# Performance work log

Measured on AMD Instinct MI355X. Metric: run time of the kernel, lower is better.

## Reference

```python
import jax, jax.numpy as jnp
import numpy as np

D_ENC = 512
D_DEC = 512
D_JOINT = D_ENC + D_DEC  # 1024
V = 1024


def setup_inputs() -> dict:
    key = jax.random.key(0)
    ks = jax.random.split(key, 8)
    s = lambda fan_in: 1.0 / np.sqrt(fan_in)
    return {
        "encoder_output": jax.random.normal(ks[0], (8, 200, D_ENC), dtype=jnp.float32),
        "decoder_output": jax.random.normal(ks[1], (8, 50, D_DEC), dtype=jnp.float32),
        "W_enc": jax.random.uniform(ks[2], (D_JOINT, D_ENC), jnp.float32, -s(D_ENC), s(D_ENC)),
        "b_enc": jax.random.uniform(ks[3], (D_JOINT,), jnp.float32, -s(D_ENC), s(D_ENC)),
        "W_dec": jax.random.uniform(ks[4], (D_JOINT, D_DEC), jnp.float32, -s(D_DEC), s(D_DEC)),
        "b_dec": jax.random.uniform(ks[5], (D_JOINT,), jnp.float32, -s(D_DEC), s(D_DEC)),
        "W_fc": jax.random.uniform(ks[6], (V, D_JOINT), jnp.float32, -s(D_JOINT), s(D_JOINT)),
        "b_fc": jax.random.uniform(ks[7], (V,), jnp.float32, -s(D_JOINT), s(D_JOINT)),
    }


def reference(encoder_output, decoder_output, W_enc, b_enc, W_dec, b_dec, W_fc, b_fc):
    # enc: (B, T, D_JOINT); dec: (B, U, D_JOINT)
    enc = jnp.einsum('btd,jd->btj', encoder_output, W_enc) + b_enc
    dec = jnp.einsum('bud,jd->buj', decoder_output, W_dec) + b_dec
    # broadcast join: (B, T, U, D_JOINT)
    combined = enc[:, :, None, :] + dec[:, None, :, :]
    logits = jnp.einsum('btuj,vj->btuv', jnp.tanh(combined), W_fc) + b_fc
    return jax.nn.log_softmax(logits, axis=-1)
```

## Files before the change

### kernel.cpp

```cpp
#include <hip/hip_runtime.h>
#include <hip/hip_bf16.h>
#include <hip/hip_fp8.h>

#define TT 200
#define UU 50
#define BB 8
#define DJ 1024
#define DE 512
#define VV 1024
#define M_TOTAL (BB*TT*UU)
#define MB 80
#define NITER 32
#define WINV (1.0f/32.0f)

typedef float f32x4 __attribute__((ext_vector_type(4)));

__device__ __forceinline__ float fast_tanh(float x) {
    float e = __expf(2.f * x);
    return 1.f - 2.f / (e + 1.f);
}

__device__ __forceinline__ unsigned char f2fp8(float x) {
    return __hip_fp8_e4m3(x).__x;
}

__device__ __forceinline__ unsigned long long tanh_pack_fp8(float4 e0, float4 e1, float4 d0, float4 d1) {
    unsigned long long r;
    r  = (unsigned long long)f2fp8(fast_tanh(e0.x + d0.x));
    r |= (unsigned long long)f2fp8(fast_tanh(e0.y + d0.y)) << 8;
    r |= (unsigned long long)f2fp8(fast_tanh(e0.z + d0.z)) << 16;
    r |= (unsigned long long)f2fp8(fast_tanh(e0.w + d0.w)) << 24;
    r |= (unsigned long long)f2fp8(fast_tanh(e1.x + d1.x)) << 32;
    r |= (unsigned long long)f2fp8(fast_tanh(e1.y + d1.y)) << 40;
    r |= (unsigned long long)f2fp8(fast_tanh(e1.z + d1.z)) << 48;
    r |= (unsigned long long)f2fp8(fast_tanh(e1.w + d1.w)) << 56;
    return r;
}

__global__ __launch_bounds__(256) void k_prep(const float* __restrict__ enc,
                                              const float* __restrict__ dec,
                                              const float* __restrict__ W_enc,
                                              const float* __restrict__ b_enc,
                                              const float* __restrict__ W_dec,
                                              const float* __restrict__ b_dec,
                                              const float* __restrict__ W_fc,
                                              float* __restrict__ encp,
                                              float* __restrict__ decp,
                                              unsigned char* __restrict__ wfc8) {
    const int bx = blockIdx.x, by = blockIdx.y;
    const int tid = threadIdx.x;
    if (bx >= 125) {
        const int wid = (bx - 125) * 4 + by;
        #pragma unroll
        for (int r = 0; r < 2; ++r) {
            const int G = wid * 512 + r * 256 + tid;
            const int gk = G >> 10, n = G & 1023;
            const float* src = W_fc + (size_t)n * DJ + gk * 8;
            float4 a = *(const float4*)(src);
            float4 b = *(const float4*)(src + 4);
            unsigned long long rr;
            rr  = (unsigned long long)f2fp8(a.x * 32.f);
            rr |= (unsigned long long)f2fp8(a.y * 32.f) << 8;
            rr |= (unsigned long long)f2fp8(a.z * 32.f) << 16;
            rr |= (unsigned long long)f2fp8(a.w * 32.f) << 24;
            rr |= (unsigned long long)f2fp8(b.x * 32.f) << 32;
            rr |= (unsigned long long)f2fp8(b.y * 32.f) << 40;
            rr |= (unsigned long long)f2fp8(b.z * 32.f) << 48;
            rr |= (unsigned long long)f2fp8(b.w * 32.f) << 56;
            *(unsigned long long*)(wfc8 + (size_t)G * 8) = rr;
        }
        return;
    }
    __shared__ float in_s[16][DE];
    const bool isDec = bx >= 100;
    const float* in  = isDec ? dec   : enc;
    const float* W   = isDec ? W_dec : W_enc;
    const float* bia = isDec ? b_dec : b_enc;
    float* out       = isDec ? decp  : encp;
    const int NR     = isDec ? (BB*UU) : (BB*TT);
    const int m0 = (isDec ? (bx - 100) : bx) * 16;
    #pragma unroll
    for (int it = 0; it < 8; ++it) {
        int idx = tid + it * 256;
        int r = idx >> 7, c = (idx & 127) << 2;
        *(float4*)&in_s[r][c] = *(const float4*)(in + (size_t)(m0 + r) * DE + c);
    }
    __syncthreads();
    const int j = by * 256 + tid;
    const float4* wr = (const float4*)(W + (size_t)j * DE);
    float acc[16];
    #pragma unroll
    for (int r = 0; r < 16; ++r) acc[r] = 0.f;
    for (int d4 = 0; d4 < DE / 4; ++d4) {
        float4 w = wr[d4];
        #pragma unroll
        for (int r = 0; r < 16; ++r) {
            float4 x = *(const float4*)&in_s[r][d4 << 2];
            acc[r] += x.x * w.x + x.y * w.y + x.z * w.z + x.w * w.w;
        }
    }
    float bv = bia[j];
    const int gk = j >> 3, kl = j & 7;
    #pragma unroll
    for (int r = 0; r < 16; ++r)
        out[((size_t)gk * NR + (m0 + r)) * 8 + kl] = acc[r] + bv;
}

__global__ __launch_bounds__(512, 2) void k_joint(const float* __restrict__ encp,
                                                  const float* __restrict__ decp,
                                                  const unsigned char* __restrict__ wfc8,
                                                  const float* __restrict__ bfc,
                                                  float* __restrict__ out) {
    __shared__ unsigned char As[81920];
    __shared__ float red[8][MB];

    const int tid = threadIdx.x;
    const int wave = tid >> 6, lane = tid & 63;
    const int g = lane >> 4, ln = lane & 15;
    const int bid = blockIdx.x;
    const int m0 = bid * MB;

    for (int r = 0; r < 20; ++r) {
        const int gidx = r * 512 + tid;
        const int gkf = gidx / MB;
        const int m = gidx - gkf * MB;
        const int mrow = m0 + m;
        const int b = mrow / (TT * UU);
        const int rem = mrow - b * (TT * UU);
        const int t = rem / UU;
        const int u = rem - t * UU;
        const float* ep = encp + ((size_t)gkf * (BB * TT) + b * TT + t) * 8;
        const float* dp = decp + ((size_t)gkf * (BB * UU) + b * UU + u) * 8;
        float4 e0 = *(const float4*)(ep);
        float4 e1 = *(const float4*)(ep + 4);
        float4 d0 = *(const float4*)(dp);
        float4 d1 = *(const float4*)(dp + 4);
        *(unsigned long long*)&As[(size_t)gidx * 8] = tanh_pack_fp8(e0, e1, d0, d1);
    }

    f32x4 acc[5][8];
    #pragma unroll
    for (int mf = 0; mf < 5; ++mf)
        #pragma unroll
        for (int nf = 0; nf < 8; ++nf)
            acc[mf][nf] = (f32x4){0.f, 0.f, 0.f, 0.f};

    __syncthreads();

    const unsigned char* bp = wfc8 + g * 8192 + (wave * 128 + ln) * 8;
    const unsigned char* ap = As + (g * MB + ln) * 8;

    #pragma unroll
    for (int t = 0; t < NITER; ++t) {
        long afr[5];
        #pragma unroll
        for (int mf = 0; mf < 5; ++mf)
            afr[mf] = *(const long*)(ap + t * 2560 + mf * 128);
        #pragma unroll
        for (int nf = 0; nf < 8; ++nf) {
            long bfr = *(const long*)(bp + (size_t)t * 32768 + nf * 128);
            #pragma unroll
            for (int mf = 0; mf < 5; ++mf)
                acc[mf][nf] = __builtin_amdgcn_mfma_f32_16x16x32_fp8_fp8(afr[mf], bfr, acc[mf][nf], 0, 0, 0);
        }
    }

    float bv[8];
    #pragma unroll
    for (int nf = 0; nf < 8; ++nf) bv[nf] = bfc[wave * 128 + nf * 16 + ln];
    #pragma unroll
    for (int mf = 0; mf < 5; ++mf)
        #pragma unroll
        for (int nf = 0; nf < 8; ++nf)
            #pragma unroll
            for (int j = 0; j < 4; ++j)
                acc[mf][nf][j] = acc[mf][nf][j] * WINV + bv[nf];

    float rmx[5][4];
    #pragma unroll
    for (int mf = 0; mf < 5; ++mf)
        #pragma unroll
        for (int j = 0; j < 4; ++j) {
            float mx = -3.0e38f;
            #pragma unroll
            for (int nf = 0; nf < 8; ++nf) mx = fmaxf(mx, acc[mf][nf][j]);
            #pragma unroll
            for (int s = 1; s < 16; s <<= 1) mx = fmaxf(mx, __shfl_xor(mx, s));
            rmx[mf][j] = mx;
        }
    if (ln == 0) {
        #pragma unroll
        for (int mf = 0; mf < 5; ++mf)
            #pragma unroll
            for (int j = 0; j < 4; ++j)
                red[wave][mf * 16 + g * 4 + j] = rmx[mf][j];
    }
    __syncthreads();
    #pragma unroll
    for (int mf = 0; mf < 5; ++mf)
        #pragma unroll
        for (int j = 0; j < 4; ++j) {
            const int r = mf * 16 + g * 4 + j;
            float mx = red[0][r];
            #pragma unroll
            for (int w = 1; w < 8; ++w) mx = fmaxf(mx, red[w][r]);
            rmx[mf][j] = mx;
        }
    __syncthreads();

    float rsm[5][4];
    #pragma unroll
    for (int mf = 0; mf < 5; ++mf)
        #pragma unroll
        for (int j = 0; j < 4; ++j) {
            float s = 0.f;
            #pragma unroll
            for (int nf = 0; nf < 8; ++nf) s += __expf(acc[mf][nf][j] - rmx[mf][j]);
            #pragma unroll
            for (int t2 = 1; t2 < 16; t2 <<= 1) s += __shfl_xor(s, t2);
            rsm[mf][j] = s;
        }
    if (ln == 0) {
        #pragma unroll
        for (int mf = 0; mf < 5; ++mf)
            #pragma unroll
            for (int j = 0; j < 4; ++j)
                red[wave][mf * 16 + g * 4 + j] = rsm[mf][j];
    }
    __syncthreads();
    #pragma unroll
    for (int mf = 0; mf < 5; ++mf)
        #pragma unroll
        for (int j = 0; j < 4; ++j) {
            const int r = mf * 16 + g * 4 + j;
            float s = 0.f;
            #pragma unroll
            for (int w = 0; w < 8; ++w) s += red[w][r];
            const float lse = rmx[mf][j] + __logf(s);
            float* op = out + (size_t)(m0 + r) * VV + wave * 128 + ln;
            #pragma unroll
            for (int nf = 0; nf < 8; ++nf)
                __builtin_nontemporal_store(acc[mf][nf][j] - lse, op + nf * 16);
        }
}

extern "C" void kernel_launch(void* const* d_in, const int* in_sizes, int n_in,
                              void* d_out, int out_size, void* d_ws, size_t ws_size,
                              hipStream_t stream) {
    const float* enc   = (const float*)d_in[0];
    const float* dec   = (const float*)d_in[1];
    const float* W_enc = (const float*)d_in[2];
    const float* b_enc = (const float*)d_in[3];
    const float* W_dec = (const float*)d_in[4];
    const float* b_dec = (const float*)d_in[5];
    const float* W_fc  = (const float*)d_in[6];
    const float* b_fc  = (const float*)d_in[7];
    float* out = (float*)d_out;

    float* encp = (float*)d_ws;
    float* decp = encp + (size_t)BB * TT * DJ;
    unsigned char* wfc8 = (unsigned char*)(decp + (size_t)BB * UU * DJ);

    k_prep<<<dim3(189, 4), 256, 0, stream>>>(enc, dec, W_enc, b_enc, W_dec, b_dec, W_fc,
                                             encp, decp, wfc8);
    k_joint<<<M_TOTAL / MB, 512, 0, stream>>>(encp, decp, wfc8, b_fc, out);
}
```

Before: 335.6 us.

## Enlarge row tile to 128 and split vocab into two passes with online softmax

Each block now covers 128 rows instead of 80 and computes the vocab dimension in two halves of 512. The accumulator stays near the same register footprint, and each B fragment load is reused across 8 M-fragments instead of 5. The softmax is merged across the halves online: the first half's raw logits go to global memory, then are read back and corrected once the final log-sum-exp is known. In exchange the A tile grows to 128KB of LDS, which likely allows only one block per CU, and the first half's output costs an extra global write and read.

```diff
diff --git a/kernel.cpp b/kernel.cpp
--- a/kernel.cpp
+++ b/kernel.cpp
@@ -9,8 +9,8 @@
 #define DE 512
 #define VV 1024
 #define M_TOTAL (BB*TT*UU)
-#define MB 80
-#define NITER 32
+#define MB 128
+#define NBLK 625
 #define WINV (1.0f/32.0f)
 
 typedef float f32x4 __attribute__((ext_vector_type(4)));
@@ -111,8 +111,9 @@
                                                   const unsigned char* __restrict__ wfc8,
                                                   const float* __restrict__ bfc,
                                                   float* __restrict__ out) {
-    __shared__ unsigned char As[81920];
+    __shared__ unsigned char As[131072];
     __shared__ float red[8][MB];
+    __shared__ float m0s[MB], s0s[MB], lsem[MB], lsef[MB];
 
     const int tid = threadIdx.x;
     const int wave = tid >> 6, lane = tid & 63;
@@ -120,10 +121,10 @@
     const int bid = blockIdx.x;
     const int m0 = bid * MB;
 
-    for (int r = 0; r < 20; ++r) {
+    for (int r = 0; r < 32; ++r) {
         const int gidx = r * 512 + tid;
-        const int gkf = gidx / MB;
-        const int m = gidx - gkf * MB;
+        const int gkf = gidx >> 7;
+        const int m = gidx & 127;
         const int mrow = m0 + m;
         const int b = mrow / (TT * UU);
         const int rem = mrow - b * (TT * UU);
@@ -137,110 +138,173 @@
         float4 d1 = *(const float4*)(dp + 4);
         *(unsigned long long*)&As[(size_t)gidx * 8] = tanh_pack_fp8(e0, e1, d0, d1);
     }
-
-    f32x4 acc[5][8];
-    #pragma unroll
-    for (int mf = 0; mf < 5; ++mf)
-        #pragma unroll
-        for (int nf = 0; nf < 8; ++nf)
+    __syncthreads();
+
+    const unsigned char* ap = As + g * 1024 + ln * 8;
+    const unsigned char* bp = wfc8 + g * 8192 + wave * 512 + ln * 8;
+
+    f32x4 acc[8][4];
+
+#define KLOOP(H)                                                                          \
+    do {                                                                                  \
+        _Pragma("unroll")                                                                 \
+        for (int kb = 0; kb < 32; ++kb) {                                                 \
+            long afr[8];                                                                  \
+            _Pragma("unroll")                                                             \
+            for (int mf = 0; mf < 8; ++mf)                                                \
+                afr[mf] = *(const long*)(ap + kb * 4096 + mf * 128);                      \
+            _Pragma("unroll")                                                             \
+            for (int nf = 0; nf < 4; ++nf) {                                              \
+                long bfr = *(const long*)(bp + (H) * 4096 + (size_t)kb * 32768 + nf * 128); \
+                _Pragma("unroll")                                                         \
+                for (int mf = 0; mf < 8; ++mf)                                            \
+                    acc[mf][nf] = __builtin_amdgcn_mfma_f32_16x16x32_fp8_fp8(             \
+                        afr[mf], bfr, acc[mf][nf], 0, 0, 0);                              \
+            }                                                                             \
+        }                                                                                 \
+    } while (0)
+
+    #pragma unroll
+    for (int mf = 0; mf < 8; ++mf)
+        #pragma unroll
+        for (int nf = 0; nf < 4; ++nf)
             acc[mf][nf] = (f32x4){0.f, 0.f, 0.f, 0.f};
-
-    __syncthreads();
-
-    const unsigned char* bp = wfc8 + g * 8192 + (wave * 128 + ln) * 8;
-    const unsigned char* ap = As + (g * MB + ln) * 8;
-
-    #pragma unroll
-    for (int t = 0; t < NITER; ++t) {
-        long afr[5];
-        #pragma unroll
-        for (int mf = 0; mf < 5; ++mf)
-            afr[mf] = *(const long*)(ap + t * 2560 + mf * 128);
-        #pragma unroll
-        for (int nf = 0; nf < 8; ++nf) {
-            long bfr = *(const long*)(bp + (size_t)t * 32768 + nf * 128);
-            #pragma unroll
-            for (int mf = 0; mf < 5; ++mf)
-                acc[mf][nf] = __builtin_amdgcn_mfma_f32_16x16x32_fp8_fp8(afr[mf], bfr, acc[mf][nf], 0, 0, 0);
-        }
-    }
-
-    float bv[8];
-    #pragma unroll
-    for (int nf = 0; nf < 8; ++nf) bv[nf] = bfc[wave * 128 + nf * 16 + ln];
-    #pragma unroll
-    for (int mf = 0; mf < 5; ++mf)
-        #pragma unroll
-        for (int nf = 0; nf < 8; ++nf)
-            #pragma unroll
-            for (int j = 0; j < 4; ++j)
-                acc[mf][nf][j] = acc[mf][nf][j] * WINV + bv[nf];
-
-    float rmx[5][4];
-    #pragma unroll
-    for (int mf = 0; mf < 5; ++mf)
-        #pragma unroll
-        for (int j = 0; j < 4; ++j) {
-            float mx = -3.0e38f;
-            #pragma unroll
-            for (int nf = 0; nf < 8; ++nf) mx = fmaxf(mx, acc[mf][nf][j]);
+    KLOOP(0);
+
+    {
+        float bv[4];
+        #pragma unroll
+        for (int nf = 0; nf < 4; ++nf) bv[nf] = bfc[wave * 64 + nf * 16 + ln];
+        #pragma unroll
+        for (int mf = 0; mf < 8; ++mf)
+            #pragma unroll
+            for (int nf = 0; nf < 4; ++nf)
+                #pragma unroll
+                for (int j = 0; j < 4; ++j)
+                    acc[mf][nf][j] = acc[mf][nf][j] * WINV + bv[nf];
+    }
+    #pragma unroll
+    for (int mf = 0; mf < 8; ++mf)
+        #pragma unroll
+        for (int j = 0; j < 4; ++j) {
+            float mx = fmaxf(fmaxf(acc[mf][0][j], acc[mf][1][j]), fmaxf(acc[mf][2][j], acc[mf][3][j]));
             #pragma unroll
             for (int s = 1; s < 16; s <<= 1) mx = fmaxf(mx, __shfl_xor(mx, s));
-            rmx[mf][j] = mx;
-        }
-    if (ln == 0) {
-        #pragma unroll
-        for (int mf = 0; mf < 5; ++mf)
-            #pragma unroll
-            for (int j = 0; j < 4; ++j)
-                red[wave][mf * 16 + g * 4 + j] = rmx[mf][j];
-    }
-    __syncthreads();
-    #pragma unroll
-    for (int mf = 0; mf < 5; ++mf)
+            if (ln == 0) red[wave][mf * 16 + g * 4 + j] = mx;
+        }
+    __syncthreads();
+    if (tid < MB) {
+        float m = red[0][tid];
+        #pragma unroll
+        for (int w = 1; w < 8; ++w) m = fmaxf(m, red[w][tid]);
+        m0s[tid] = m;
+    }
+    __syncthreads();
+    #pragma unroll
+    for (int mf = 0; mf < 8; ++mf)
         #pragma unroll
         for (int j = 0; j < 4; ++j) {
             const int r = mf * 16 + g * 4 + j;
-            float mx = red[0][r];
-            #pragma unroll
-            for (int w = 1; w < 8; ++w) mx = fmaxf(mx, red[w][r]);
-            rmx[mf][j] = mx;
-        }
-    __syncthreads();
-
-    float rsm[5][4];
-    #pragma unroll
-    for (int mf = 0; mf < 5; ++mf)
-        #pragma unroll
-        for (int j = 0; j < 4; ++j) {
-            float s = 0.f;
-            #pragma unroll
-            for (int nf = 0; nf < 8; ++nf) s += __expf(acc[mf][nf][j] - rmx[mf][j]);
+            const float rm = m0s[r];
+            float s = __expf(acc[mf][0][j] - rm) + __expf(acc[mf][1][j] - rm)
+                    + __expf(acc[mf][2][j] - rm) + __expf(acc[mf][3][j] - rm);
             #pragma unroll
             for (int t2 = 1; t2 < 16; t2 <<= 1) s += __shfl_xor(s, t2);
-            rsm[mf][j] = s;
-        }
-    if (ln == 0) {
-        #pragma unroll
-        for (int mf = 0; mf < 5; ++mf)
-            #pragma unroll
-            for (int j = 0; j < 4; ++j)
-                red[wave][mf * 16 + g * 4 + j] = rsm[mf][j];
-    }
-    __syncthreads();
-    #pragma unroll
-    for (int mf = 0; mf < 5; ++mf)
+            if (ln == 0) red[wave][r] = s;
+        }
+    __syncthreads();
+    if (tid < MB) {
+        float s = 0.f;
+        #pragma unroll
+        for (int w = 0; w < 8; ++w) s += red[w][tid];
+        s0s[tid] = s;
+    }
+    #pragma unroll
+    for (int mf = 0; mf < 8; ++mf)
         #pragma unroll
         for (int j = 0; j < 4; ++j) {
             const int r = mf * 16 + g * 4 + j;
-            float s = 0.f;
-            #pragma unroll
-            for (int w = 0; w < 8; ++w) s += red[w][r];
-            const float lse = rmx[mf][j] + __logf(s);
-            float* op = out + (size_t)(m0 + r) * VV + wave * 128 + ln;
-            #pragma unroll
-            for (int nf = 0; nf < 8; ++nf)
-                __builtin_nontemporal_store(acc[mf][nf][j] - lse, op + nf * 16);
+            float* op = out + (size_t)(m0 + r) * VV + wave * 64 + ln;
+            #pragma unroll
+            for (int nf = 0; nf < 4; ++nf)
+                op[nf * 16] = acc[mf][nf][j];
+        }
+    __syncthreads();
+
+    #pragma unroll
+    for (int mf = 0; mf < 8; ++mf)
+        #pragma unroll
+        for (int nf = 0; nf < 4; ++nf)
+            acc[mf][nf] = (f32x4){0.f, 0.f, 0.f, 0.f};
+    KLOOP(1);
+#undef KLOOP
+
+    {
+        float bv[4];
+        #pragma unroll
+        for (int nf = 0; nf < 4; ++nf) bv[nf] = bfc[512 + wave * 64 + nf * 16 + ln];
+        #pragma unroll
+        for (int mf = 0; mf < 8; ++mf)
+            #pragma unroll
+            for (int nf = 0; nf < 4; ++nf)
+                #pragma unroll
+                for (int j = 0; j < 4; ++j)
+                    acc[mf][nf][j] = acc[mf][nf][j] * WINV + bv[nf];
+    }
+    #pragma unroll
+    for (int mf = 0; mf < 8; ++mf)
+        #pragma unroll
+        for (int j = 0; j < 4; ++j) {
+            float mx = fmaxf(fmaxf(acc[mf][0][j], acc[mf][1][j]), fmaxf(acc[mf][2][j], acc[mf][3][j]));
+            #pragma unroll
+            for (int s = 1; s < 16; s <<= 1) mx = fmaxf(mx, __shfl_xor(mx, s));
+            if (ln == 0) red[wave][mf * 16 + g * 4 + j] = mx;
+        }
+    __syncthreads();
+    if (tid < MB) {
+        float m1 = red[0][tid];
+        #pragma unroll
+        for (int w = 1; w < 8; ++w) m1 = fmaxf(m1, red[w][tid]);
+        lsem[tid] = fmaxf(m0s[tid], m1);
+    }
+    __syncthreads();
+    #pragma unroll
+    for (int mf = 0; mf < 8; ++mf)
+        #pragma unroll
+        for (int j = 0; j < 4; ++j) {
+            const int r = mf * 16 + g * 4 + j;
+            const float rm = lsem[r];
+            float s = __expf(acc[mf][0][j] - rm) + __expf(acc[mf][1][j] - rm)
+                    + __expf(acc[mf][2][j] - rm) + __expf(acc[mf][3][j] - rm);
+            #pragma unroll
+            for (int t2 = 1; t2 < 16; t2 <<= 1) s += __shfl_xor(s, t2);
+            if (ln == 0) red[wave][r] = s;
+        }
+    __syncthreads();
+    if (tid < MB) {
+        float s = s0s[tid] * __expf(m0s[tid] - lsem[tid]);
+        #pragma unroll
+        for (int w = 0; w < 8; ++w) s += red[w][tid];
+        lsef[tid] = lsem[tid] + __logf(s);
+    }
+    __syncthreads();
+
+    #pragma unroll
+    for (int mf = 0; mf < 8; ++mf)
+        #pragma unroll
+        for (int j = 0; j < 4; ++j) {
+            const int r = mf * 16 + g * 4 + j;
+            const float L = lsef[r];
+            float* op1 = out + (size_t)(m0 + r) * VV + 512 + wave * 64 + ln;
+            #pragma unroll
+            for (int nf = 0; nf < 4; ++nf)
+                __builtin_nontemporal_store(acc[mf][nf][j] - L, op1 + nf * 16);
+            float* op0 = out + (size_t)(m0 + r) * VV + wave * 64 + ln;
+            #pragma unroll
+            for (int nf = 0; nf < 4; ++nf) {
+                float v = op0[nf * 16];
+                __builtin_nontemporal_store(v - L, op0 + nf * 16);
+            }
         }
 }
 
@@ -263,5 +327,5 @@
 
     k_prep<<<dim3(189, 4), 256, 0, stream>>>(enc, dec, W_enc, b_enc, W_dec, b_dec, W_fc,
                                              encp, decp, wfc8);
-    k_joint<<<M_TOTAL / MB, 512, 0, stream>>>(encp, decp, wfc8, b_fc, out);
-}
+    k_joint<<<NBLK, 512, 0, stream>>>(encp, decp, wfc8, b_fc, out);
+}
```

Result: slower. 569.2 us (+69.6%).

## Stage fp8 W_fc tiles into per-wave LDS double buffers via async global_load_lds

Applied to the files above, without the earlier changes.

Instead of each lane reading B fragments straight from global memory inside the MFMA loop, each wave asynchronously copies the next k-step's W_fc slab into its own double-buffered LDS region using global_load_lds. It waits with s_waitcnt vmcnt before consuming the current slab. The goal is to hide global and L2 latency behind the MFMA work and to get wide, coalesced 16-byte loads. In exchange it uses about 66 KB more LDS per block and relies on hand-written vmcnt accounting, which needs care to stay correct.

```diff
diff --git a/kernel.cpp b/kernel.cpp
--- a/kernel.cpp
+++ b/kernel.cpp
@@ -12,6 +12,9 @@
 #define MB 80
 #define NITER 32
 #define WINV (1.0f/32.0f)
+#define ROWPAD 1040
+#define BUFHALF (4*ROWPAD)
+#define BUFW (2*BUFHALF)
 
 typedef float f32x4 __attribute__((ext_vector_type(4)));
 
@@ -35,6 +38,12 @@
     r |= (unsigned long long)f2fp8(fast_tanh(e1.z + d1.z)) << 48;
     r |= (unsigned long long)f2fp8(fast_tanh(e1.w + d1.w)) << 56;
     return r;
+}
+
+__device__ __forceinline__ void gload_lds16(const unsigned char* g, unsigned char* l) {
+    __builtin_amdgcn_global_load_lds(
+        (const __attribute__((address_space(1))) unsigned int*)(const void*)g,
+        (__attribute__((address_space(3))) unsigned int*)(void*)l, 16, 0, 0);
 }
 
 __global__ __launch_bounds__(256) void k_prep(const float* __restrict__ enc,
@@ -112,6 +121,7 @@
                                                   const float* __restrict__ bfc,
                                                   float* __restrict__ out) {
     __shared__ unsigned char As[81920];
+    __shared__ unsigned char Bw[8 * BUFW];
     __shared__ float red[8][MB];
 
     const int tid = threadIdx.x;
@@ -147,18 +157,34 @@
 
     __syncthreads();
 
-    const unsigned char* bp = wfc8 + g * 8192 + (wave * 128 + ln) * 8;
-    const unsigned char* ap = As + (g * MB + ln) * 8;
+    const unsigned char* gsrc = wfc8 + wave * 1024 + lane * 16;
+    unsigned char* ldst = Bw + wave * BUFW + lane * 16;
+    const unsigned char* brd = Bw + wave * BUFW + g * ROWPAD + ln * 8;
+    const unsigned char* ap = As + g * 640 + ln * 8;
+
+    #pragma unroll
+    for (int gg = 0; gg < 4; ++gg)
+        gload_lds16(gsrc + (size_t)gg * 8192, ldst + gg * ROWPAD);
 
     #pragma unroll
     for (int t = 0; t < NITER; ++t) {
+        const int cur = t & 1, nxt = cur ^ 1;
+        if (t < NITER - 1) {
+            #pragma unroll
+            for (int gg = 0; gg < 4; ++gg)
+                gload_lds16(gsrc + (size_t)((t + 1) * 4 + gg) * 8192,
+                            ldst + nxt * BUFHALF + gg * ROWPAD);
+            asm volatile("s_waitcnt vmcnt(4)" ::: "memory");
+        } else {
+            asm volatile("s_waitcnt vmcnt(0)" ::: "memory");
+        }
         long afr[5];
         #pragma unroll
         for (int mf = 0; mf < 5; ++mf)
             afr[mf] = *(const long*)(ap + t * 2560 + mf * 128);
         #pragma unroll
         for (int nf = 0; nf < 8; ++nf) {
-            long bfr = *(const long*)(bp + (size_t)t * 32768 + nf * 128);
+            long bfr = *(const long*)(brd + cur * BUFHALF + nf * 128);
             #pragma unroll
             for (int mf = 0; mf < 5; ++mf)
                 acc[mf][nf] = __builtin_amdgcn_mfma_f32_16x16x32_fp8_fp8(afr[mf], bfr, acc[mf][nf], 0, 0, 0);
```

Measured after the change: 339.5 us. About the same (+1.2%).
